# Performance work log

Measured on AMD Instinct MI355X. Metric: run time of the kernel, lower is better.

The kernel has to match this reference:

```python
import jax, jax.numpy as jnp
import numpy as np

C, H, NP = 256, 8, 64      # d_model, nhead, num_prototype
DH, DK = C // H, NP // H   # value head dim, prototype head dim
EPS = 1e-6


def layer_norm(x, g, b, eps=1e-5):
    m = jnp.mean(x, axis=-1, keepdims=True)
    v = jnp.mean((x - m) ** 2, axis=-1, keepdims=True)
    return (x - m) * jax.lax.rsqrt(v + eps) * g + b


def linear_attention(Q, K, V, q_mask=None, kv_mask=None):
    # LoFTR kernelized linear attention, feature map elu(x)+1
    Q = jax.nn.elu(Q) + 1.0
    K = jax.nn.elu(K) + 1.0
    if q_mask is not None:
        Q = Q * q_mask[:, :, None, None].astype(Q.dtype)
    if kv_mask is not None:
        m = kv_mask[:, :, None, None].astype(K.dtype)
        K = K * m
        V = V * m
    v_len = V.shape[1]
    Vn = V / v_len
    KV = jnp.einsum('nshd,nshv->nhdv', K, Vn)                      # [n,h,d,v]
    Z = 1.0 / (jnp.einsum('nlhd,nhd->nlh', Q, K.sum(axis=1)) + EPS)
    return jnp.einsum('nlhd,nhdv,nlh->nlhv', Q, KV, Z) * v_len


def detr_decoder(query, feat, feat_mask, p):
    bs = query.shape[0]
    # query self-attention
    qq = (query @ p['dWqq']).reshape(bs, -1, H, DH)
    qk = (query @ p['dWqk']).reshape(bs, -1, H, DH)
    qv = (query @ p['dWqv']).reshape(bs, -1, H, DH)
    msg = linear_attention(qq, qk, qv, None, None).reshape(bs, -1, C) @ p['dWqm']
    msg = layer_norm(query + msg, p['dln1_g'], p['dln1_b'])
    # prototype cross-attention over feat
    mq = (msg @ p['dWpq']).reshape(bs, -1, H, DH)
    fk = (feat @ p['dWpk']).reshape(bs, -1, H, DH)
    fv = (feat @ p['dWpv']).reshape(bs, -1, H, DH)
    proto = linear_attention(mq, fk, fv, None, feat_mask).reshape(bs, -1, C) @ p['dWpm']
    proto = layer_norm(msg + proto, p['dln2_g'], p['dln2_b'])
    ffn = jax.nn.relu(proto @ p['dWf1']) @ p['dWf2']
    return layer_norm(proto + ffn, p['dln3_g'], p['dln3_b'])


def forward(x, source, x_mask, source_mask, p):
    bs = x.shape[0]
    q = x @ p['Wq']
    k = source @ p['Wk']
    # DETR-style prototype extraction from x
    proto_in = jnp.broadcast_to(p['proto_q'][None], (bs, NP, C))
    prototype = detr_decoder(proto_in, x, x_mask, p)
    pp = prototype @ p['Wqp']
    pk = prototype @ p['Wkp']
    # re-project q/k through prototypes: [n,l,K]
    q = jnp.einsum('nlc,nkc->nlk', q, pp)
    k = jnp.einsum('nsc,nkc->nsk', k, pk)
    q = jnp.where(x_mask[:, :, None], q, -jnp.inf)
    q = jax.nn.softmax(q, axis=1) * jnp.nan_to_num(jax.nn.softmax(q, axis=2))
    k = jnp.where(source_mask[:, :, None], k, -jnp.inf)
    k = jax.nn.softmax(k, axis=1) * jnp.nan_to_num(jax.nn.softmax(k, axis=2))
    q = q.reshape(bs, -1, H, DK)
    k = k.reshape(bs, -1, H, DK)
    v = (source @ p['Wv']).reshape(bs, -1, H, DH)
    msg = linear_attention(q, k, v, x_mask, source_mask)
    msg = msg.reshape(bs, -1, C) @ p['Wmerge']
    msg = layer_norm(msg, p['ln1_g'], p['ln1_b'])
    msg = jax.nn.relu(jnp.concatenate([x, msg], axis=-1) @ p['Wmlp1']) @ p['Wmlp2']
    msg = layer_norm(msg, p['ln2_g'], p['ln2_b'])
    return x + msg


def setup_inputs() -> dict:
    key = jax.random.key(0)
    ks = jax.random.split(key, 24)
    def W(i, shape, scale):
        return jax.random.normal(ks[i], shape, jnp.float32) * scale
    s = 1.0 / np.sqrt(C).astype(np.float32)
    s2 = 1.0 / np.sqrt(2 * C).astype(np.float32)
    B, L, S = 8, 4800, 4800
    ones_c = jnp.ones((C,), jnp.float32)
    zeros_c = jnp.zeros((C,), jnp.float32)
    return {
        'x': W(0, (B, L, C), 1.0),
        'source': W(1, (B, S, C), 1.0),
        'x_mask': jnp.ones((B, L), dtype=bool),
        'source_mask': jnp.ones((B, S), dtype=bool),
        'Wq': W(2, (C, C), s), 'Wk': W(3, (C, C), s), 'Wv': W(4, (C, C), s),
        'Wqp': W(5, (C, C), s), 'Wkp': W(6, (C, C), s),
        'Wmerge': W(7, (C, C), s),
        'Wmlp1': W(8, (2 * C, 2 * C), s2), 'Wmlp2': W(9, (2 * C, C), s2),
        'ln1_g': ones_c, 'ln1_b': zeros_c,
        'ln2_g': ones_c, 'ln2_b': zeros_c,
        'proto_q': W(10, (NP, C), 1.0),
        'dWqq': W(11, (C, C), s), 'dWqk': W(12, (C, C), s),
        'dWqv': W(13, (C, C), s), 'dWqm': W(14, (C, C), s),
        'dln1_g': ones_c, 'dln1_b': zeros_c,
        'dWpq': W(15, (C, C), s), 'dWpk': W(16, (C, C), s),
        'dWpv': W(17, (C, C), s), 'dWpm': W(18, (C, C), s),
        'dln2_g': ones_c, 'dln2_b': zeros_c,
        'dWf1': W(19, (C, C), s), 'dWf2': W(20, (C, C), s),
        'dln3_g': ones_c, 'dln3_b': zeros_c,
    }


def reference(x, source, x_mask, source_mask, Wq, Wk, Wv, Wqp, Wkp, Wmerge,
              Wmlp1, Wmlp2, ln1_g, ln1_b, ln2_g, ln2_b, proto_q,
              dWqq, dWqk, dWqv, dWqm, dln1_g, dln1_b,
              dWpq, dWpk, dWpv, dWpm, dln2_g, dln2_b,
              dWf1, dWf2, dln3_g, dln3_b):
    p = dict(Wq=Wq, Wk=Wk, Wv=Wv, Wqp=Wqp, Wkp=Wkp, Wmerge=Wmerge,
             Wmlp1=Wmlp1, Wmlp2=Wmlp2, ln1_g=ln1_g, ln1_b=ln1_b,
             ln2_g=ln2_g, ln2_b=ln2_b, proto_q=proto_q,
             dWqq=dWqq, dWqk=dWqk, dWqv=dWqv, dWqm=dWqm,
             dln1_g=dln1_g, dln1_b=dln1_b,
             dWpq=dWpq, dWpk=dWpk, dWpv=dWpv, dWpm=dWpm,
             dln2_g=dln2_g, dln2_b=dln2_b,
             dWf1=dWf1, dWf2=dWf2, dln3_g=dln3_g, dln3_b=dln3_b)
    return forward(x, source, x_mask, source_mask, p)
```

## Files before the change

### kernel.cpp

```cpp
#include <hip/hip_runtime.h>
#include <hip/hip_bf16.h>

typedef unsigned short u16;
typedef __bf16 bf16x8 __attribute__((ext_vector_type(8)));
typedef float  f32x4  __attribute__((ext_vector_type(4)));

__device__ __forceinline__ float b2f(u16 u){
  union{ unsigned int i; float f; } a; a.i = ((unsigned int)u)<<16; return a.f;
}
__device__ __forceinline__ u16 f2b(float f){
  __hip_bfloat16 h = __float2bfloat16(f);
  u16 r; __builtin_memcpy(&r, &h, 2); return r;
}
__device__ __forceinline__ int imin(int a,int b){ return a<b?a:b; }

__device__ __forceinline__ void gl_lds16(const void* g, void* l){
  __builtin_amdgcn_global_load_lds(
      (const __attribute__((address_space(1))) void*)g,
      (__attribute__((address_space(3))) void*)l, 16, 0, 0);
}
__device__ __forceinline__ void vm_drain(){
  asm volatile("s_waitcnt vmcnt(0)" ::: "memory");
}
__device__ __forceinline__ void vm_wait4(){
  asm volatile("s_waitcnt vmcnt(4)" ::: "memory");
}

template<int KD, int OUTMODE, bool CAT, int NSEL>
__global__ __launch_bounds__(256) void gemm128(
    const u16* __restrict__ A, const u16* __restrict__ A2, const u16* __restrict__ A3,
    const u16* __restrict__ Wt, const u16* __restrict__ Wt2, const u16* __restrict__ Wt3,
    float* __restrict__ Cf, u16* __restrict__ Cb, u16* __restrict__ Cb2, u16* __restrict__ Cb3,
    int NDIM, int aoff)
{
  __shared__ u16 At[3][128*32];
  __shared__ u16 Bt[3][128*32];
  const int tid = threadIdx.x;
  const int ny = gridDim.y, nz = gridDim.z;
  const int NB = gridDim.x*ny*nz;
  const int L  = blockIdx.x + gridDim.x*(blockIdx.y + ny*blockIdx.z);
  const int cpx = NB >> 3;
  const int wkid = (L & 7)*cpx + (L >> 3);
  const int nc = ny*nz;
  const int bx = wkid / nc;
  const int cc_ = wkid - bx*nc;
  const int by = cc_ % ny;
  const int bz = cc_ / ny;

  const u16* Aa = (NSEL>=3 && bz==2) ? A3 : A;
  const u16* W  = (NSEL>=2 && bz==1) ? Wt2 : ((NSEL>=3 && bz==2) ? Wt3 : Wt);
  u16* Cbo      = (NSEL>=2 && bz==1) ? Cb2 : ((NSEL>=3 && bz==2) ? Cb3 : Cb);
  const int w = tid>>6, lane = tid&63;
  const int q4 = lane>>4, l15 = lane&15;
  const int wr = w>>1, wc = w&1;
  const int rstage = lane>>2;
  const int kcol = (((lane&3) ^ ((lane>>2)&3))<<3);
  const size_t arow0 = (size_t)(aoff + bx*128);
  const int n0 = by*128;

  f32x4 acc[4][4];
  #pragma unroll
  for (int i=0;i<4;i++)
    #pragma unroll
    for (int j=0;j<4;j++){ acc[i][j][0]=0.f; acc[i][j][1]=0.f; acc[i][j][2]=0.f; acc[i][j][3]=0.f; }

  auto stage = [&](int k0, int buf){
    #pragma unroll
    for (int j=0;j<2;j++){
      const int trow = w*32 + j*16 + rstage;
      const u16* ga;
      if (CAT){
        ga = (k0<256) ? (A  + (arow0+trow)*256 + k0 + kcol)
                      : (A2 + (arow0+trow)*256 + (k0-256) + kcol);
      } else {
        ga = Aa + (arow0+trow)*(size_t)KD + k0 + kcol;
      }
      gl_lds16(ga, &At[buf][(w*32+j*16)*32]);
      const u16* gb = W + (size_t)(n0 + trow)*KD + k0 + kcol;
      gl_lds16(gb, &Bt[buf][(w*32+j*16)*32]);
    }
  };

  constexpr int NK = KD/32;
  stage(0, 0);
  stage(32, 1);
  vm_wait4();
  __builtin_amdgcn_s_barrier();
  int cb = 0;
  for (int t=0; t<NK; ++t){
    if (t+2 < NK){
      int sbuf = cb ? cb-1 : 2;
      stage((t+2)*32, sbuf);
    }
    bf16x8 af[4], bv[4];
    #pragma unroll
    for (int i=0;i<4;i++){
      __builtin_memcpy(&af[i], &At[cb][(wr*64 + i*16 + l15)*32 + ((q4^(l15&3))<<3)], 16);
      __builtin_memcpy(&bv[i], &Bt[cb][(wc*64 + i*16 + l15)*32 + ((q4^(l15&3))<<3)], 16);
    }
    #pragma unroll
    for (int i=0;i<4;i++)
      #pragma unroll
      for (int j=0;j<4;j++)
        acc[i][j] = __builtin_amdgcn_mfma_f32_16x16x32_bf16(af[i], bv[j], acc[i][j], 0,0,0);
    if (t+1 < NK){
      if (t+2 < NK) vm_wait4(); else vm_drain();
      __builtin_amdgcn_s_barrier();
      cb = (cb==2)? 0 : cb+1;
    }
  }
  #pragma unroll
  for (int i=0;i<4;i++){
    const int row0 = bx*128 + wr*64 + i*16 + q4*4;
    #pragma unroll
    for (int j=0;j<4;j++){
      const int col = n0 + wc*64 + j*16 + l15;
      #pragma unroll
      for (int r=0;r<4;r++){
        float v = acc[i][j][r];
        size_t idx = (size_t)(row0+r)*NDIM + col;
        if (OUTMODE==0) Cf[idx]=v;
        else if (OUTMODE==1) Cbo[idx]=f2b(v);
        else Cbo[idx]=f2b(v>0.f?v:0.f);
      }
    }
  }
}

__global__ __launch_bounds__(256) void cvt_split2(
    const float* __restrict__ inA, u16* __restrict__ ohA, u16* __restrict__ olA,
    const float* __restrict__ inB, u16* __restrict__ ohB, u16* __restrict__ olB, int n){
  int i = (blockIdx.x*256 + threadIdx.x)*4;
  const float* in; u16 *oh, *ol; int j;
  if (i < n){ in=inA; oh=ohA; ol=olA; j=i; }
  else      { in=inB; oh=ohB; ol=olB; j=i-n; }
  float4 f = *(const float4*)(in+j);
  float v[4]={f.x,f.y,f.z,f.w};
  #pragma unroll
  for (int t=0;t<4;t++){ u16 h=f2b(v[t]); oh[j+t]=h; ol[j+t]=f2b(v[t]-b2f(h)); }
}

__global__ __launch_bounds__(256) void wtrans4(
    const float* __restrict__ W0, const float* __restrict__ W1,
    const float* __restrict__ W2, const float* __restrict__ W3,
    u16* __restrict__ T0, u16* __restrict__ T1,
    u16* __restrict__ T2, u16* __restrict__ T3)
{
  const int g = blockIdx.y;
  const float* W = g==0?W0:(g==1?W1:(g==2?W2:W3));
  u16* T = g==0?T0:(g==1?T1:(g==2?T2:T3));
  int idx = blockIdx.x*256 + threadIdx.x;
  int nn = idx>>8, kk = idx&255;
  T[idx] = f2b(W[(size_t)kk*256 + nn]);
}

__global__ __launch_bounds__(256) void wtrans2(
    const float* __restrict__ W1, u16* __restrict__ T1,
    const float* __restrict__ W2, u16* __restrict__ T2)
{
  int idx = blockIdx.x*256 + threadIdx.x;
  if (idx < 512*512){
    int nn = idx>>9, kk = idx&511;
    T1[idx] = f2b(W1[(size_t)kk*512 + nn]);
  } else {
    int j = idx - 512*512;
    int nn = j>>9, kk = j&511;
    T2[j] = f2b(W2[(size_t)kk*256 + nn]);
  }
}

__global__ __launch_bounds__(256) void warm7(
    const float* __restrict__ W0, const float* __restrict__ W1,
    const float* __restrict__ W2, const float* __restrict__ W3,
    const float* __restrict__ W4, const float* __restrict__ W5,
    const float* __restrict__ W6, float* __restrict__ scratch)
{
  const int slice = blockIdx.x >> 3;
  const int wsel = slice >> 6;
  const int off = ((slice & 63)<<8) + threadIdx.x;
  const float* W = wsel==0?W0:wsel==1?W1:wsel==2?W2:wsel==3?W3:wsel==4?W4:wsel==5?W5:W6;
  float4 v = ((const float4*)W)[off];
  float s = v.x+v.y+v.z+v.w;
  if (s == 1234567.891f) scratch[blockIdx.x] = s;
}

__global__ __launch_bounds__(256) void gemm_logits2(
    const u16* __restrict__ Ah0, const u16* __restrict__ Al0,
    const u16* __restrict__ Bh0, const u16* __restrict__ Bl0,
    float* __restrict__ O0,
    const u16* __restrict__ Ah1, const u16* __restrict__ Al1,
    const u16* __restrict__ Bh1, const u16* __restrict__ Bl1,
    float* __restrict__ O1)
{
  __shared__ u16 SA[3][64*32], SAL[3][64*32], SB[3][64*32], SBL[3][64*32];
  const int tid=threadIdx.x, bx=blockIdx.x;
  const int sel = blockIdx.y;
  const u16* Ah = sel? Ah1:Ah0;  const u16* Al = sel? Al1:Al0;
  const u16* BhT= sel? Bh1:Bh0;  const u16* BlT= sel? Bl1:Bl0;
  float* Out = sel? O1:O0;
  const int w=tid>>6, lane=tid&63, q4=lane>>4, l15=lane&15;
  const int bloc = bx/75;
  const u16* bh_ = BhT + (size_t)bloc*16384;
  const u16* bl_ = BlT + (size_t)bloc*16384;
  const size_t arow0 = (size_t)bx*64;
  const int rsub = lane>>2;
  const int csub = (((lane&3) ^ ((lane>>2)&3))<<3);
  f32x4 acc[4];
  #pragma unroll
  for (int t=0;t<4;t++){ acc[t][0]=0.f; acc[t][1]=0.f; acc[t][2]=0.f; acc[t][3]=0.f; }

  auto stage = [&](int k0, int buf){
    #pragma unroll
    for (int i=0;i<4;i++){
      const int row = i*16 + rsub;
      if (w==0)      gl_lds16(Ah + (arow0+row)*256 + k0 + csub, &SA [buf][i*16*32]);
      else if (w==1) gl_lds16(Al + (arow0+row)*256 + k0 + csub, &SAL[buf][i*16*32]);
      else if (w==2) gl_lds16(bh_ + (size_t)row*256 + k0 + csub, &SB [buf][i*16*32]);
      else           gl_lds16(bl_ + (size_t)row*256 + k0 + csub, &SBL[buf][i*16*32]);
    }
  };

  stage(0, 0);
  stage(32, 1);
  vm_wait4();
  __builtin_amdgcn_s_barrier();
  int cb = 0;
  for (int t=0;t<8;++t){
    if (t+2 < 8){
      int sbuf = cb ? cb-1 : 2;
      stage((t+2)*32, sbuf);
    }
    bf16x8 ah, al;
    __builtin_memcpy(&ah, &SA [cb][(w*16+l15)*32 + ((q4^(l15&3))<<3)], 16);
    __builtin_memcpy(&al, &SAL[cb][(w*16+l15)*32 + ((q4^(l15&3))<<3)], 16);
    #pragma unroll
    for (int nt=0;nt<4;nt++){
      bf16x8 bh, bl;
      __builtin_memcpy(&bh, &SB [cb][(nt*16+l15)*32 + ((q4^(l15&3))<<3)], 16);
      __builtin_memcpy(&bl, &SBL[cb][(nt*16+l15)*32 + ((q4^(l15&3))<<3)], 16);
      acc[nt] = __builtin_amdgcn_mfma_f32_16x16x32_bf16(ah, bh, acc[nt], 0,0,0);
      acc[nt] = __builtin_amdgcn_mfma_f32_16x16x32_bf16(ah, bl, acc[nt], 0,0,0);
      acc[nt] = __builtin_amdgcn_mfma_f32_16x16x32_bf16(al, bh, acc[nt], 0,0,0);
    }
    if (t+1 < 8){
      if (t+2 < 8) vm_wait4(); else vm_drain();
      __builtin_amdgcn_s_barrier();
      cb = (cb==2)? 0 : cb+1;
    }
  }
  #pragma unroll
  for (int nt=0;nt<4;nt++)
    #pragma unroll
    for (int r=0;r<4;r++)
      Out[(arow0 + w*16 + q4*4 + r)*64 + nt*16 + l15] = acc[nt][r];
}

template<int DKT, bool ELU, bool KF32, bool KSM>
__global__ __launch_bounds__(256) void la_reduce_mfma(
    const void* __restrict__ Kv, int kstride, const u16* __restrict__ Vv,
    float* __restrict__ KV, float* __restrict__ Ks, int Skv,
    const float* __restrict__ cmax, const float* __restrict__ csum)
{
  constexpr int PAD = 136;
  constexpr int MROW = (DKT<16)?16:DKT;
  __shared__ u16 Klt[MROW*PAD];
  __shared__ u16 Vlt[32*PAD];
  __shared__ float Ksl[DKT];
  const int tid = threadIdx.x;
  const int bh = blockIdx.y; const int b = bh>>3, h = bh&7;
  const int s0 = blockIdx.x*256;
  if (tid < DKT) Ksl[tid] = 0.f;

  const int w = tid>>6, lane = tid&63, q4 = lane>>4, l15 = lane&15;
  constexpr int NT = (DKT==32)?4:2;
  const int tileid = w % NT;
  const int mt = (DKT==32)? (tileid>>1) : 0;
  const int nt = (DKT==32)? (tileid&1) : tileid;
  constexpr int KPER = (DKT==32)?4:2;
  const int k0w = (w/NT)*KPER;

  const int kd = tid & (DKT-1);
  const int ksrow = tid / DKT;
  const int ksstep = 256/DKT;
  const int vv = tid & 31, vsrow = tid >> 5;

  f32x4 acc; acc[0]=0.f; acc[1]=0.f; acc[2]=0.f; acc[3]=0.f;
  float kacc = 0.f;

  for (int cc=0; cc<2; cc++){
    const int sc0 = s0 + cc*128;
    if constexpr (KSM){
      #pragma unroll
      for (int t=0; t<4; t++){
        int s = ksrow + t*32;
        float xv = 0.f;
        if (sc0+s < Skv){
          const float* rowp = (const float*)Kv + ((size_t)b*Skv + sc0+s)*64;
          float vals[8];
          #pragma unroll
          for (int j=0;j<8;j++) vals[j] = rowp[kd + 8*j];
          float m = vals[0];
          #pragma unroll
          for (int j=1;j<8;j++) m = fmaxf(m, vals[j]);
          #pragma unroll
          for (int off=1;off<8;off<<=1) m = fmaxf(m, __shfl_xor(m, off));
          float ssum = 0.f;
          #pragma unroll
          for (int j=0;j<8;j++) ssum += __expf(vals[j]-m);
          #pragma unroll
          for (int off=1;off<8;off<<=1) ssum += __shfl_xor(ssum, off);
          float vneed = vals[0];
          #pragma unroll
          for (int j=1;j<8;j++) if (h==j) vneed = vals[j];
          const int np = h*8 + kd;
          float cs = __expf(vneed - cmax[(size_t)b*64+np]) / csum[(size_t)b*64+np];
          xv = (__expf(vneed-m)/ssum)*cs + 1.f;
        }
        Klt[kd*PAD + s] = f2b(xv);
        kacc += xv;
      }
    } else {
      #pragma unroll
      for (int t=0; t<DKT/2; t++){
        int s = ksrow + t*ksstep;
        float xv = 0.f;
        if (sc0+s < Skv){
          size_t gi = ((size_t)b*Skv + sc0+s)*kstride + h*DKT + kd;
          float kk = KF32 ? ((const float*)Kv)[gi] : b2f(((const u16*)Kv)[gi]);
          xv = ELU ? (kk>0.f? kk+1.f : __expf(kk)) : kk+1.f;
        }
        Klt[kd*PAD + s] = f2b(xv);
        kacc += xv;
      }
    }
    if (DKT==8){
      for (int i=tid; i<8*128; i+=256){ int rr=8+(i>>7), s=i&127; Klt[rr*PAD+s]=0; }
    }
    #pragma unroll
    for (int t=0; t<16; t++){
      int s = vsrow + t*8;
      u16 raw = 0;
      if (sc0+s < Skv) raw = Vv[((size_t)b*Skv + sc0+s)*256 + h*32 + vv];
      Vlt[vv*PAD + s] = raw;
    }
    __syncthreads();
    #pragma unroll
    for (int kk=0; kk<KPER; kk++){
      int ks = k0w + kk;
      bf16x8 af, bv;
      __builtin_memcpy(&af, &Klt[(mt*16+l15)*PAD + ks*32 + q4*8], 16);
      __builtin_memcpy(&bv, &Vlt[(nt*16+l15)*PAD + ks*32 + q4*8], 16);
      acc = __builtin_amdgcn_mfma_f32_16x16x32_bf16(af, bv, acc, 0,0,0);
    }
    __syncthreads();
  }
  #pragma unroll
  for (int r=0;r<4;r++){
    int row = q4*4 + r;
    if (DKT==32 || row < 8){
      int dg = mt*16 + row;
      atomicAdd(&KV[((size_t)bh*DKT + dg)*32 + nt*16 + l15], acc[r]);
    }
  }
  atomicAdd(&Ksl[kd], kacc);
  __syncthreads();
  if (tid < DKT) atomicAdd(&Ks[(size_t)bh*DKT + tid], Ksl[tid]);
}

__global__ __launch_bounds__(256) void small_gemm3(
    const float* __restrict__ A,
    const float* __restrict__ W0, const float* __restrict__ W1, const float* __restrict__ W2,
    float* __restrict__ O0, float* __restrict__ O1, float* __restrict__ O2,
    int mode, int amask)
{
  __shared__ float Alds[4][256];
  const int g = blockIdx.x>>7;
  const float* W = g==0?W0:(g==1?W1:W2);
  float* Of = g==0?O0:(g==1?O1:O2);
  const int tid=threadIdx.x; const int r0=(blockIdx.x&127)*4;
  for (int i=tid;i<1024;i+=256){ int r=i>>8, c=i&255;
    Alds[r][c]=A[(size_t)((r0+r)&amask)*256+c]; }
  __syncthreads();
  float a0=0.f,a1=0.f,a2=0.f,a3=0.f;
  for (int k=0;k<256;k++){
    float w=W[(size_t)k*256+tid];
    a0+=Alds[0][k]*w; a1+=Alds[1][k]*w; a2+=Alds[2][k]*w; a3+=Alds[3][k]*w;
  }
  float accs[4]={a0,a1,a2,a3};
  #pragma unroll
  for (int r=0;r<4;r++){
    size_t idx=(size_t)(r0+r)*256+tid; float v=accs[r];
    if (mode==1) v = v>0.f?v:0.f;
    Of[idx]=v;
  }
}

template<int R>
__global__ __launch_bounds__(256) void decoder_chain(
    const float* __restrict__ S1, const float* __restrict__ proq,
    const float* __restrict__ KV1, const float* __restrict__ Ks1,
    const float* __restrict__ KV2, const float* __restrict__ Ks2,
    const float* __restrict__ dWqm, const float* __restrict__ dl1g, const float* __restrict__ dl1b,
    const float* __restrict__ dWpq,
    const float* __restrict__ dWpm, const float* __restrict__ dl2g, const float* __restrict__ dl2b,
    const float* __restrict__ dWf1, const float* __restrict__ dWf2,
    const float* __restrict__ dl3g, const float* __restrict__ dl3b,
    const float* __restrict__ Wqp, const float* __restrict__ Wkp,
    float* __restrict__ ppf, float* __restrict__ pkf)
{
  __shared__ float KVl[8*32*32];
  __shared__ float Ksl[8*32];
  __shared__ float rowA[R][256];
  __shared__ float rowB[R][256];
  __shared__ float red[4][R], red2[4][R];
  const int tid = threadIdx.x;
  const int r0g = blockIdx.x*R;
  const int b = r0g >> 6;
  const int h = tid>>5, vv = tid&31;
  const int w_ = tid>>6, ln_ = tid&63;

  auto gemmR = [&](float (*Ain)[256], const float* __restrict__ W, float* out){
    float a[R];
    #pragma unroll
    for (int r=0;r<R;r++) a[r]=0.f;
    float wv[16], wn[16];
    #pragma unroll
    for (int u=0;u<16;u++) wn[u]=0.f;
    #pragma unroll
    for (int u=0;u<16;u++) wv[u]=W[(size_t)u*256+tid];
    for (int k0=0;k0<256;k0+=16){
      if (k0+16<256){
        #pragma unroll
        for (int u=0;u<16;u++) wn[u]=W[(size_t)(k0+16+u)*256+tid];
      }
      #pragma unroll
      for (int u=0;u<16;u++){
        #pragma unroll
        for (int r=0;r<R;r++) a[r]+=Ain[r][k0+u]*wv[u];
      }
      #pragma unroll
      for (int u=0;u<16;u++) wv[u]=wn[u];
    }
    #pragma unroll
    for (int r=0;r<R;r++) out[r]=a[r];
  };
  auto lnR = [&](float* v, const float* __restrict__ g, const float* __restrict__ be,
                 float (*Out)[256]){
    float s[R];
    #pragma unroll
    for (int r=0;r<R;r++) s[r]=v[r];
    #pragma unroll
    for (int off=32;off;off>>=1){
      #pragma unroll
      for (int r=0;r<R;r++) s[r]+=__shfl_xor(s[r],off);
    }
    if (ln_==0){
      #pragma unroll
      for (int r=0;r<R;r++) red[w_][r]=s[r];
    }
    __syncthreads();
    float mean[R];
    #pragma unroll
    for (int r=0;r<R;r++) mean[r]=(red[0][r]+red[1][r]+red[2][r]+red[3][r])*(1.f/256.f);
    float q[R];
    #pragma unroll
    for (int r=0;r<R;r++){ float d=v[r]-mean[r]; q[r]=d*d; }
    #pragma unroll
    for (int off=32;off;off>>=1){
      #pragma unroll
      for (int r=0;r<R;r++) q[r]+=__shfl_xor(q[r],off);
    }
    if (ln_==0){
      #pragma unroll
      for (int r=0;r<R;r++) red2[w_][r]=q[r];
    }
    __syncthreads();
    const float gg=g[tid], bb=be[tid];
    #pragma unroll
    for (int r=0;r<R;r++){
      float var=(red2[0][r]+red2[1][r]+red2[2][r]+red2[3][r])*(1.f/256.f);
      Out[r][tid]=(v[r]-mean[r])*rsqrtf(var+1e-5f)*gg+bb;
    }
    __syncthreads();
  };
  auto applyR = [&](float (*Q)[256], float (*Out)[256]){
    float res[R];
    #pragma unroll
    for (int r=0;r<R;r++){
      float z=0.f,o=0.f;
      #pragma unroll 8
      for (int d=0;d<32;d++){
        float q = Q[r][h*32+d];
        q = q>0.f? q+1.f : __expf(q);
        z += q*Ksl[h*32+d];
        o += q*KVl[(h*32+d)*32+vv];
      }
      res[r]=o/(z+1e-6f);
    }
    __syncthreads();
    #pragma unroll
    for (int r=0;r<R;r++) Out[r][h*32+vv]=res[r];
    __syncthreads();
  };

  for (int i=tid;i<8192;i+=256) KVl[i]=KV1[(size_t)b*8192+i];
  Ksl[tid]=Ks1[(size_t)b*256+tid];
  for (int i=tid;i<R*256;i+=256){ int r=i>>8,c=i&255; rowA[r][c]=S1[(size_t)(r0g+r)*256+c]; }
  __syncthreads();
  applyR(rowA,rowB);
  float v[R], v2[R];
  gemmR(rowB,dWqm,v);
  #pragma unroll
  for (int r=0;r<R;r++) v[r]+=proq[(size_t)((r0g+r)&63)*256+tid];
  lnR(v,dl1g,dl1b,rowA);
  gemmR(rowA,dWpq,v2);
  #pragma unroll
  for (int r=0;r<R;r++) rowB[r][tid]=v2[r];
  for (int i=tid;i<8192;i+=256) KVl[i]=KV2[(size_t)b*8192+i];
  Ksl[tid]=Ks2[(size_t)b*256+tid];
  __syncthreads();
  applyR(rowB,rowB);
  gemmR(rowB,dWpm,v);
  #pragma unroll
  for (int r=0;r<R;r++) v[r]+=rowA[r][tid];
  lnR(v,dl2g,dl2b,rowA);
  gemmR(rowA,dWf1,v);
  #pragma unroll
  for (int r=0;r<R;r++) rowB[r][tid]=v[r]>0.f?v[r]:0.f;
  __syncthreads();
  gemmR(rowB,dWf2,v);
  #pragma unroll
  for (int r=0;r<R;r++) v[r]+=rowA[r][tid];
  lnR(v,dl3g,dl3b,rowA);
  gemmR(rowA,Wqp,v);
  gemmR(rowA,Wkp,v2);
  #pragma unroll
  for (int r=0;r<R;r++){
    ppf[(size_t)(r0g+r)*256+tid]=v[r];
    pkf[(size_t)(r0g+r)*256+tid]=v2[r];
  }
}

__global__ __launch_bounds__(256) void proj_mat2(
    const float* __restrict__ Wa, const float* __restrict__ Pa,
    u16* __restrict__ Mha, u16* __restrict__ Mla,
    const float* __restrict__ Wb, const float* __restrict__ Pb,
    u16* __restrict__ Mhb, u16* __restrict__ Mlb)
{
  __shared__ float PL[64][256];
  const float* W = blockIdx.z? Wb:Wa;
  const float* P = blockIdx.z? Pb:Pa;
  u16* MhT = blockIdx.z? Mhb:Mha;
  u16* MlT = blockIdx.z? Mlb:Mla;
  const int b = blockIdx.x, c0 = blockIdx.y*16, tid = threadIdx.x;
  for (int i=tid;i<16384;i+=256){ int row=i>>8, col=i&255;
    PL[row][col] = P[(size_t)(b*64+row)*256 + col]; }
  __syncthreads();
  const int np = tid&63, cl = tid>>6;
  #pragma unroll
  for (int rr=0;rr<4;rr++){
    int ci = cl + rr*4;
    float acc=0.f;
    for (int j=0;j<256;j++) acc += W[(size_t)(c0+ci)*256+j]*PL[np][j];
    size_t idx = (size_t)b*16384 + (size_t)np*256 + (c0+ci);
    u16 h=f2b(acc); MhT[idx]=h; MlT[idx]=f2b(acc-b2f(h));
  }
}

template<int DKT, bool ELU>
__global__ __launch_bounds__(256) void la_reduce(
    const float* __restrict__ Kv, int kstride, const float* __restrict__ Vv,
    float* __restrict__ KV, float* __restrict__ Ks, int Skv, int clen)
{
  __shared__ float Kl[64*DKT];
  __shared__ float Vl[64*32];
  const int b = blockIdx.y>>3, h = blockIdx.y&7;
  const int tid=threadIdx.x;
  const int s0 = blockIdx.x*clen; const int s1 = imin(s0+clen, Skv);
  const int d0 = tid>>5, vvv = tid&31;
  float acc[DKT/8], kac[DKT/8];
  #pragma unroll
  for (int p=0;p<DKT/8;p++){ acc[p]=0.f; kac[p]=0.f; }
  for (int sc=s0; sc<s1; sc+=64){
    int ns = imin(64, s1-sc);
    for (int i=tid;i<ns*DKT;i+=256){ int s=i/DKT, d=i-s*DKT;
      float xv = Kv[((size_t)b*Skv + sc+s)*kstride + h*DKT + d];
      Kl[s*DKT+d] = ELU ? (xv>0.f? xv+1.f : __expf(xv)) : xv+1.f; }
    for (int i=tid;i<ns*32;i+=256){ int s=i>>5, c=i&31;
      Vl[s*32+c] = Vv[((size_t)b*Skv+sc+s)*256 + h*32 + c]; }
    __syncthreads();
    for (int s=0;s<ns;s++){
      float vval = Vl[s*32+vvv];
      #pragma unroll
      for (int p=0;p<DKT/8;p++){ float kk=Kl[s*DKT + d0+8*p]; acc[p]+=kk*vval; kac[p]+=kk; }
    }
    __syncthreads();
  }
  #pragma unroll
  for (int p=0;p<DKT/8;p++)
    atomicAdd(&KV[(((size_t)b*8+h)*DKT + d0+8*p)*32 + vvv], acc[p]);
  if (vvv==0){
    #pragma unroll
    for (int p=0;p<DKT/8;p++)
      atomicAdd(&Ks[((size_t)b*8+h)*DKT + d0+8*p], kac[p]);
  }
}

template<int DKT, bool ELU, bool OUTBF, bool QSM>
__global__ __launch_bounds__(256) void la_apply(
    const float* __restrict__ Qsrc, const float* __restrict__ KV,
    const float* __restrict__ Ks, int Lq, float* __restrict__ outf, u16* __restrict__ outb,
    const float* __restrict__ cmax, const float* __restrict__ csum)
{
  __shared__ float KVl[8*DKT*32];
  __shared__ float Ksl[8*DKT];
  __shared__ float Ql[16*8*DKT];
  const int b = blockIdx.y; const int r0 = blockIdx.x*16;
  const int tid = threadIdx.x;
  const float* KVb = KV + (size_t)b*8*DKT*32;
  for (int i=tid;i<8*DKT*32;i+=256) KVl[i]=KVb[i];
  for (int i=tid;i<8*DKT;i+=256) Ksl[i]=Ks[(size_t)b*8*DKT + i];
  if constexpr (QSM){
    const int wv = tid>>6, ln = tid&63;
    #pragma unroll
    for (int rr=0;rr<4;rr++){
      const int r = wv*4+rr;
      float v = Qsrc[((size_t)b*Lq + r0 + r)*64 + ln];
      float m = v;
      #pragma unroll
      for (int off=32;off;off>>=1) m = fmaxf(m, __shfl_xor(m,off));
      float e = __expf(v-m);
      float s = e;
      #pragma unroll
      for (int off=32;off;off>>=1) s += __shfl_xor(s,off);
      float cs = __expf(v - cmax[(size_t)b*64+ln]) / csum[(size_t)b*64+ln];
      Ql[r*64+ln] = (e/s)*cs;
    }
  } else {
    for (int i=tid;i<16*8*DKT;i+=256){ int r=i/(8*DKT); int c=i-r*(8*DKT);
        Ql[i] = Qsrc[((size_t)b*Lq + r0 + r)*(8*DKT) + c]; }
  }
  __syncthreads();
  const int h = tid>>5, vv = tid&31;
  for (int r=0;r<16;r++){
    float z=0.f, o=0.f;
    #pragma unroll
    for (int d=0; d<DKT; d++){
      float q = Ql[r*8*DKT + h*DKT + d];
      q = ELU ? (q>0.f? q+1.f : __expf(q)) : q+1.f;
      z += q*Ksl[h*DKT+d];
      o += q*KVl[(h*DKT+d)*32 + vv];
    }
    float res = o/(z+1e-6f);
    size_t idx = ((size_t)b*Lq + r0+r)*256 + h*32+vv;
    if (OUTBF) outb[idx]=f2b(res); else outf[idx]=res;
  }
}

template<int MODE, bool ABF>
__global__ __launch_bounds__(256) void ln_kernel(
  const void* __restrict__ Av, const float* __restrict__ resid,
  const float* __restrict__ g, const float* __restrict__ be,
  float* __restrict__ Of, u16* __restrict__ Ob, const float* __restrict__ xadd,
  float* __restrict__ Ox)
{
  const int tid = threadIdx.x;
  const size_t row = (size_t)blockIdx.x*4 + (tid>>6);
  const int lane = tid&63;
  const int c0 = lane<<2;
  const size_t gi = row*256 + c0;
  float v[4];
  if (MODE==1 || ABF){
    ushort4 u = *(const ushort4*)((const u16*)Av + gi);
    v[0]=b2f(u.x); v[1]=b2f(u.y); v[2]=b2f(u.z); v[3]=b2f(u.w);
  } else {
    float4 f = *(const float4*)((const float*)Av + gi);
    v[0]=f.x; v[1]=f.y; v[2]=f.z; v[3]=f.w;
  }
  if (MODE==0){
    float4 r = *(const float4*)(resid + gi);
    v[0]+=r.x; v[1]+=r.y; v[2]+=r.z; v[3]+=r.w;
  }
  float s = v[0]+v[1]+v[2]+v[3];
  #pragma unroll
  for (int off=32;off;off>>=1) s += __shfl_xor(s,off);
  const float mean = s*(1.f/256.f);
  float d[4]; float qq=0.f;
  #pragma unroll
  for (int i=0;i<4;i++){ d[i]=v[i]-mean; qq += d[i]*d[i]; }
  #pragma unroll
  for (int off=32;off;off>>=1) qq += __shfl_xor(qq,off);
  const float rstd = rsqrtf(qq*(1.f/256.f)+1e-5f);
  const float4 gv = *(const float4*)(g+c0);
  const float4 bv = *(const float4*)(be+c0);
  float y[4];
  y[0]=d[0]*rstd*gv.x+bv.x; y[1]=d[1]*rstd*gv.y+bv.y;
  y[2]=d[2]*rstd*gv.z+bv.z; y[3]=d[3]*rstd*gv.w+bv.w;
  if (MODE==0){
    *(float4*)(Of+gi) = make_float4(y[0],y[1],y[2],y[3]);
  } else if (MODE==1){
    ushort4 o; o.x=f2b(y[0]); o.y=f2b(y[1]); o.z=f2b(y[2]); o.w=f2b(y[3]);
    *(ushort4*)(Ob+gi)=o;
  } else {
    const float4 xa = *(const float4*)(xadd+gi);
    *(float4*)(Ox+gi) = make_float4(xa.x+y[0], xa.y+y[1], xa.z+y[2], xa.w+y[3]);
  }
}

__global__ __launch_bounds__(256) void col_stats(
    const float* __restrict__ logits0, float* __restrict__ cmax0, float* __restrict__ csum0,
    const float* __restrict__ logits1, float* __restrict__ cmax1, float* __restrict__ csum1)
{
  int np = blockIdx.x, b = blockIdx.y;
  const float* logits = blockIdx.z? logits1:logits0;
  float* cmax = blockIdx.z? cmax1:cmax0;
  float* csum = blockIdx.z? csum1:csum0;
  const float* base = logits + ((size_t)b*4800)*64 + np;
  int tid = threadIdx.x;
  float vloc[19];
  float m = -3.0e38f;
  #pragma unroll
  for (int i=0;i<19;i++){ int l = tid + i*256;
    float v = (l<4800)? base[(size_t)l*64] : -3.0e38f;
    vloc[i]=v; m = fmaxf(m,v); }
  #pragma unroll
  for (int off=32;off;off>>=1) m = fmaxf(m, __shfl_xor(m,off));
  __shared__ float red[4], red2[4];
  int w = tid>>6, ln = tid&63;
  if (ln==0) red[w]=m;
  __syncthreads();
  m = fmaxf(fmaxf(red[0],red[1]), fmaxf(red[2],red[3]));
  float s=0.f;
  #pragma unroll
  for (int i=0;i<19;i++){ int l = tid + i*256; if (l<4800) s += __expf(vloc[i]-m); }
  #pragma unroll
  for (int off=32;off;off>>=1) s += __shfl_xor(s,off);
  if (ln==0) red2[w]=s;
  __syncthreads();
  s = red2[0]+red2[1]+red2[2]+red2[3];
  if (tid==0){ cmax[b*64+np]=m; csum[b*64+np]=s; }
}

extern "C" void kernel_launch(void* const* d_in, const int* in_sizes, int n_in,
                              void* d_out, int out_size, void* d_ws, size_t ws_size,
                              hipStream_t stream) {
  (void)in_sizes; (void)n_in; (void)out_size; (void)ws_size;
  const float* x    = (const float*)d_in[0];
  const float* srcp = (const float*)d_in[1];
  const float* Wq   = (const float*)d_in[4];
  const float* Wk   = (const float*)d_in[5];
  const float* Wv   = (const float*)d_in[6];
  const float* Wqp  = (const float*)d_in[7];
  const float* Wkp  = (const float*)d_in[8];
  const float* Wmg  = (const float*)d_in[9];
  const float* Wm1  = (const float*)d_in[10];
  const float* Wm2  = (const float*)d_in[11];
  const float* ln1g = (const float*)d_in[12];
  const float* ln1b = (const float*)d_in[13];
  const float* ln2g = (const float*)d_in[14];
  const float* ln2b = (const float*)d_in[15];
  const float* proq = (const float*)d_in[16];
  const float* dWqq = (const float*)d_in[17];
  const float* dWqk = (const float*)d_in[18];
  const float* dWqv = (const float*)d_in[19];
  const float* dWqm = (const float*)d_in[20];
  const float* dl1g = (const float*)d_in[21];
  const float* dl1b = (const float*)d_in[22];
  const float* dWpq = (const float*)d_in[23];
  const float* dWpk = (const float*)d_in[24];
  const float* dWpv = (const float*)d_in[25];
  const float* dWpm = (const float*)d_in[26];
  const float* dWf1 = (const float*)d_in[29];
  const float* dWf2 = (const float*)d_in[30];
  const float* dl3g = (const float*)d_in[31];
  const float* dl3b = (const float*)d_in[32];
  const float* dl2g = (const float*)d_in[27];
  const float* dl2b = (const float*)d_in[28];

  char* p=(char*)d_ws;
  auto alloc=[&](size_t n)->char*{ char* r=p; p+=((n+255)&~(size_t)255); return r; };
  u16* xb  = (u16*)alloc(19660800);
  u16* xlo = (u16*)alloc(19660800);
  u16* sb  = (u16*)alloc(19660800);
  u16* slo = (u16*)alloc(19660800);
  u16* bufA= (u16*)alloc(19660800);
  u16* bufB= (u16*)alloc(19660800);
  u16* v0b = (u16*)alloc(19660800);
  u16* msg1b=(u16*)alloc(19660800);
  u16* h1  = (u16*)alloc(39321600);
  u16* mlp2b=(u16*)alloc(19660800);
  float* qsm=(float*)alloc(9830400);
  float* ksm=(float*)alloc(9830400);
  u16* dWpkT=(u16*)alloc(131072); u16* dWpvT=(u16*)alloc(131072);
  u16* WvT  =(u16*)alloc(131072); u16* WmgT =(u16*)alloc(131072);
  u16* Wm1T =(u16*)alloc(524288); u16* Wm2T =(u16*)alloc(262144);
  float* S0=(float*)alloc(524288); float* S1=(float*)alloc(524288);
  float* S2=(float*)alloc(524288); float* S3=(float*)alloc(524288);
  float* S4=(float*)alloc(524288); float* S5=(float*)alloc(524288);
  float* ppf=(float*)alloc(524288); float* pkf=(float*)alloc(524288);
  u16* Mqh=(u16*)alloc(262144); u16* Mql=(u16*)alloc(262144);
  u16* Mkh=(u16*)alloc(262144); u16* Mkl=(u16*)alloc(262144);
  char* z0=p;
  float* KV1=(float*)alloc(262144); float* Ks1=(float*)alloc(8192);
  float* KV2=(float*)alloc(262144); float* Ks2=(float*)alloc(8192);
  float* KVm=(float*)alloc(65536);  float* Ksm=(float*)alloc(2048);
  char* z1=p;
  float* cmq=(float*)alloc(2048); float* csq=(float*)alloc(2048);
  float* cmk=(float*)alloc(2048); float* csk=(float*)alloc(2048);
  (void)S4; (void)S5;

  u16* fk=bufA;
  u16* fv=bufB; u16* msg0b=bufB;
  float* dof=(float*)d_out;

  hipMemsetAsync(z0, 0, (size_t)(z1-z0), stream);

  dim3 blk(256);
  cvt_split2<<<dim3(19200),blk,0,stream>>>(x, xb, xlo, srcp, sb, slo, 9830400);
  wtrans4<<<dim3(256,4),blk,0,stream>>>(dWpk,dWpv,Wv,Wmg, dWpkT,dWpvT,WvT,WmgT);
  wtrans2<<<dim3(1536),blk,0,stream>>>(Wm1, Wm1T, Wm2, Wm2T);
  gemm128<256,1,false,3><<<dim3(300,2,3),blk,0,stream>>>(
      xb,nullptr,sb, dWpkT,dWpvT,WvT, nullptr, fk,fv,v0b, 256,0);
  la_reduce_mfma<32,true,false,false><<<dim3(19,64),blk,0,stream>>>(
      fk,256,fv,KV2,Ks2,4800,nullptr,nullptr);
  small_gemm3<<<dim3(384),blk,0,stream>>>(proq,dWqq,dWqk,dWqv,S1,S2,S3,0,63);
  la_reduce<32,true><<<dim3(1,64),blk,0,stream>>>(S2,256,S3,KV1,Ks1,64,64);
  warm7<<<dim3(3584),blk,0,stream>>>(dWqm,dWpq,dWpm,dWf1,dWf2,Wqp,Wkp,S0);
  decoder_chain<2><<<dim3(256),blk,0,stream>>>(
      S1,proq, KV1,Ks1, KV2,Ks2,
      dWqm,dl1g,dl1b, dWpq, dWpm,dl2g,dl2b, dWf1,dWf2,dl3g,dl3b,
      Wqp,Wkp, ppf,pkf);
  proj_mat2<<<dim3(8,16,2),blk,0,stream>>>(Wq,ppf,Mqh,Mql, Wk,pkf,Mkh,Mkl);
  gemm_logits2<<<dim3(600,2),blk,0,stream>>>(xb,xlo,Mqh,Mql,qsm, sb,slo,Mkh,Mkl,ksm);
  col_stats<<<dim3(64,8,2),blk,0,stream>>>(qsm,cmq,csq, ksm,cmk,csk);
  la_reduce_mfma<8,false,true,true><<<dim3(19,64),blk,0,stream>>>(
      ksm,64,v0b,KVm,Ksm,4800,cmk,csk);
  la_apply<8,false,true,true><<<dim3(300,8),blk,0,stream>>>(
      qsm,KVm,Ksm,4800,nullptr,msg0b,cmq,csq);
  gemm128<256,1,false,1><<<dim3(300,2),blk,0,stream>>>(
      msg0b,nullptr,nullptr, WmgT,nullptr,nullptr, nullptr, msg1b,nullptr,nullptr, 256,0);
  ln_kernel<1,false><<<dim3(9600),blk,0,stream>>>(msg1b,nullptr,ln1g,ln1b,nullptr,msg1b,nullptr,nullptr);
  gemm128<512,2,true,1><<<dim3(300,4),blk,0,stream>>>(
      xb,msg1b,nullptr, Wm1T,nullptr,nullptr, nullptr, h1,nullptr,nullptr, 512,0);
  gemm128<512,1,false,1><<<dim3(300,2),blk,0,stream>>>(
      h1,nullptr,nullptr, Wm2T,nullptr,nullptr, nullptr, mlp2b,nullptr,nullptr, 256,0);
  ln_kernel<2,true><<<dim3(9600),blk,0,stream>>>(mlp2b,nullptr,ln2g,ln2b,nullptr,nullptr,x,dof);
}
```

Measured before the change: 528.3 us.

## Split decoder chain to one row per block and fuse final two projections

The decoder_chain launch changes from two rows per block on 256 blocks to one row per block on 512 blocks, spreading the serial per-row GEMM/LayerNorm chain over more CUs. The final Wqp and Wkp projections are merged into one pass that streams both weight matrices together, so the activation row is read once. The second KV/Ks load into LDS is moved earlier so it sits before the first gemm rather than after the dWpq gemm. More blocks means the weight matrices are re-read from cache more times overall.

```diff
diff --git a/kernel.cpp b/kernel.cpp
--- a/kernel.cpp
+++ b/kernel.cpp
@@ -444,6 +444,33 @@
     #pragma unroll
     for (int r=0;r<R;r++) out[r]=a[r];
   };
+  auto gemmR2 = [&](float (*Ain)[256], const float* __restrict__ Wa,
+                    const float* __restrict__ Wb, float* oa, float* ob){
+    float a[R], bacc[R];
+    #pragma unroll
+    for (int r=0;r<R;r++){ a[r]=0.f; bacc[r]=0.f; }
+    float wa[8], wb[8], na[8], nb[8];
+    #pragma unroll
+    for (int u=0;u<8;u++){ wa[u]=Wa[(size_t)u*256+tid]; wb[u]=Wb[(size_t)u*256+tid]; }
+    for (int k0=0;k0<256;k0+=8){
+      if (k0+8<256){
+        #pragma unroll
+        for (int u=0;u<8;u++){ na[u]=Wa[(size_t)(k0+8+u)*256+tid]; nb[u]=Wb[(size_t)(k0+8+u)*256+tid]; }
+      }
+      #pragma unroll
+      for (int u=0;u<8;u++){
+        #pragma unroll
+        for (int r=0;r<R;r++){
+          float av = Ain[r][k0+u];
+          a[r]+=av*wa[u]; bacc[r]+=av*wb[u];
+        }
+      }
+      #pragma unroll
+      for (int u=0;u<8;u++){ wa[u]=na[u]; wb[u]=nb[u]; }
+    }
+    #pragma unroll
+    for (int r=0;r<R;r++){ oa[r]=a[r]; ob[r]=bacc[r]; }
+  };
   auto lnR = [&](float* v, const float* __restrict__ g, const float* __restrict__ be,
                  float (*Out)[256]){
     float s[R];
@@ -508,6 +535,8 @@
   for (int i=tid;i<R*256;i+=256){ int r=i>>8,c=i&255; rowA[r][c]=S1[(size_t)(r0g+r)*256+c]; }
   __syncthreads();
   applyR(rowA,rowB);
+  for (int i=tid;i<8192;i+=256) KVl[i]=KV2[(size_t)b*8192+i];
+  Ksl[tid]=Ks2[(size_t)b*256+tid];
   float v[R], v2[R];
   gemmR(rowB,dWqm,v);
   #pragma unroll
@@ -516,8 +545,6 @@
   gemmR(rowA,dWpq,v2);
   #pragma unroll
   for (int r=0;r<R;r++) rowB[r][tid]=v2[r];
-  for (int i=tid;i<8192;i+=256) KVl[i]=KV2[(size_t)b*8192+i];
-  Ksl[tid]=Ks2[(size_t)b*256+tid];
   __syncthreads();
   applyR(rowB,rowB);
   gemmR(rowB,dWpm,v);
@@ -532,8 +559,7 @@
   #pragma unroll
   for (int r=0;r<R;r++) v[r]+=rowA[r][tid];
   lnR(v,dl3g,dl3b,rowA);
-  gemmR(rowA,Wqp,v);
-  gemmR(rowA,Wkp,v2);
+  gemmR2(rowA,Wqp,Wkp,v,v2);
   #pragma unroll
   for (int r=0;r<R;r++){
     ppf[(size_t)(r0g+r)*256+tid]=v[r];
@@ -826,7 +852,7 @@
   small_gemm3<<<dim3(384),blk,0,stream>>>(proq,dWqq,dWqk,dWqv,S1,S2,S3,0,63);
   la_reduce<32,true><<<dim3(1,64),blk,0,stream>>>(S2,256,S3,KV1,Ks1,64,64);
   warm7<<<dim3(3584),blk,0,stream>>>(dWqm,dWpq,dWpm,dWf1,dWf2,Wqp,Wkp,S0);
-  decoder_chain<2><<<dim3(256),blk,0,stream>>>(
+  decoder_chain<1><<<dim3(512),blk,0,stream>>>(
       S1,proq, KV1,Ks1, KV2,Ks2,
       dWqm,dl1g,dl1b, dWpq, dWpm,dl2g,dl2b, dWf1,dWf2,dl3g,dl3b,
       Wqp,Wkp, ppf,pkf);
```

New measurement: 521.9 us (median of 2 runs). Within noise of the previous version (-1.2%).

## Split decoder chain to one row per block with split-K GEMV reduction

Applied to the files above, without the earlier changes.

The decoder chain kernel now handles one prototype row per block instead of two, doubling the grid to 512 blocks. Each GEMV splits K across the four waves and combines partial sums through a shared-memory buffer. The final Wqp/Wkp projections are fused into one pass over both weights, and the KV2 load into LDS is moved earlier. The aim is to shorten the serial dependency chain per block and use more CUs, at the cost of extra barriers and more total weight reads across blocks.

```diff
diff --git a/kernel.cpp b/kernel.cpp
--- a/kernel.cpp
+++ b/kernel.cpp
@@ -395,7 +395,6 @@
   }
 }
 
-template<int R>
 __global__ __launch_bounds__(256) void decoder_chain(
     const float* __restrict__ S1, const float* __restrict__ proq,
     const float* __restrict__ KV1, const float* __restrict__ Ks1,
@@ -410,135 +409,137 @@
 {
   __shared__ float KVl[8*32*32];
   __shared__ float Ksl[8*32];
-  __shared__ float rowA[R][256];
-  __shared__ float rowB[R][256];
-  __shared__ float red[4][R], red2[4][R];
+  __shared__ float rowA[256];
+  __shared__ float rowB[256];
+  __shared__ float red[4], red2[4];
+  __shared__ float gred[4][256];
   const int tid = threadIdx.x;
-  const int r0g = blockIdx.x*R;
+  const int r0g = blockIdx.x;
   const int b = r0g >> 6;
   const int h = tid>>5, vv = tid&31;
   const int w_ = tid>>6, ln_ = tid&63;
 
-  auto gemmR = [&](float (*Ain)[256], const float* __restrict__ W, float* out){
-    float a[R];
-    #pragma unroll
-    for (int r=0;r<R;r++) a[r]=0.f;
+  auto gemmS = [&](const float* Ain, const float* __restrict__ W, float& out){
+    const int kb = w_*64;
+    float a0=0.f,a1=0.f,a2=0.f,a3=0.f;
     float wv[16], wn[16];
     #pragma unroll
     for (int u=0;u<16;u++) wn[u]=0.f;
     #pragma unroll
-    for (int u=0;u<16;u++) wv[u]=W[(size_t)u*256+tid];
-    for (int k0=0;k0<256;k0+=16){
-      if (k0+16<256){
+    for (int u=0;u<16;u++) wv[u]=W[(size_t)(kb+u)*256+tid];
+    #pragma unroll
+    for (int kc=0;kc<64;kc+=16){
+      if (kc<48){
         #pragma unroll
-        for (int u=0;u<16;u++) wn[u]=W[(size_t)(k0+16+u)*256+tid];
+        for (int u=0;u<16;u++) wn[u]=W[(size_t)(kb+kc+16+u)*256+tid];
       }
       #pragma unroll
-      for (int u=0;u<16;u++){
+      for (int u=0;u<16;u+=4){
+        a0+=Ain[kb+kc+u  ]*wv[u  ];
+        a1+=Ain[kb+kc+u+1]*wv[u+1];
+        a2+=Ain[kb+kc+u+2]*wv[u+2];
+        a3+=Ain[kb+kc+u+3]*wv[u+3];
+      }
+      #pragma unroll
+      for (int u=0;u<16;u++) wv[u]=wn[u];
+    }
+    gred[w_][tid]=(a0+a1)+(a2+a3);
+    __syncthreads();
+    out = (gred[0][tid]+gred[1][tid])+(gred[2][tid]+gred[3][tid]);
+    __syncthreads();
+  };
+  auto gemmS2 = [&](const float* Ain, const float* __restrict__ Wa,
+                    const float* __restrict__ Wb, float& oa, float& ob){
+    const int kb = w_*64;
+    float a0=0.f,a1=0.f,b0=0.f,b1=0.f;
+    float wa[8], wb[8], na[8], nb[8];
+    #pragma unroll
+    for (int u=0;u<8;u++){ na[u]=0.f; nb[u]=0.f; }
+    #pragma unroll
+    for (int u=0;u<8;u++){ wa[u]=Wa[(size_t)(kb+u)*256+tid]; wb[u]=Wb[(size_t)(kb+u)*256+tid]; }
+    #pragma unroll
+    for (int kc=0;kc<64;kc+=8){
+      if (kc<56){
         #pragma unroll
-        for (int r=0;r<R;r++) a[r]+=Ain[r][k0+u]*wv[u];
+        for (int u=0;u<8;u++){ na[u]=Wa[(size_t)(kb+kc+8+u)*256+tid]; nb[u]=Wb[(size_t)(kb+kc+8+u)*256+tid]; }
       }
       #pragma unroll
-      for (int u=0;u<16;u++) wv[u]=wn[u];
-    }
-    #pragma unroll
-    for (int r=0;r<R;r++) out[r]=a[r];
+      for (int u=0;u<8;u+=2){
+        float av0=Ain[kb+kc+u], av1=Ain[kb+kc+u+1];
+        a0+=av0*wa[u]; a1+=av1*wa[u+1];
+        b0+=av0*wb[u]; b1+=av1*wb[u+1];
+      }
+      #pragma unroll
+      for (int u=0;u<8;u++){ wa[u]=na[u]; wb[u]=nb[u]; }
+    }
+    gred[w_][tid]=a0+a1;
+    __syncthreads();
+    oa = (gred[0][tid]+gred[1][tid])+(gred[2][tid]+gred[3][tid]);
+    __syncthreads();
+    gred[w_][tid]=b0+b1;
+    __syncthreads();
+    ob = (gred[0][tid]+gred[1][tid])+(gred[2][tid]+gred[3][tid]);
+    __syncthreads();
   };
-  auto lnR = [&](float* v, const float* __restrict__ g, const float* __restrict__ be,
-                 float (*Out)[256]){
-    float s[R];
-    #pragma unroll
-    for (int r=0;r<R;r++) s[r]=v[r];
-    #pragma unroll
-    for (int off=32;off;off>>=1){
-      #pragma unroll
-      for (int r=0;r<R;r++) s[r]+=__shfl_xor(s[r],off);
-    }
-    if (ln_==0){
-      #pragma unroll
-      for (int r=0;r<R;r++) red[w_][r]=s[r];
-    }
-    __syncthreads();
-    float mean[R];
-    #pragma unroll
-    for (int r=0;r<R;r++) mean[r]=(red[0][r]+red[1][r]+red[2][r]+red[3][r])*(1.f/256.f);
-    float q[R];
-    #pragma unroll
-    for (int r=0;r<R;r++){ float d=v[r]-mean[r]; q[r]=d*d; }
-    #pragma unroll
-    for (int off=32;off;off>>=1){
-      #pragma unroll
-      for (int r=0;r<R;r++) q[r]+=__shfl_xor(q[r],off);
-    }
-    if (ln_==0){
-      #pragma unroll
-      for (int r=0;r<R;r++) red2[w_][r]=q[r];
-    }
-    __syncthreads();
-    const float gg=g[tid], bb=be[tid];
-    #pragma unroll
-    for (int r=0;r<R;r++){
-      float var=(red2[0][r]+red2[1][r]+red2[2][r]+red2[3][r])*(1.f/256.f);
-      Out[r][tid]=(v[r]-mean[r])*rsqrtf(var+1e-5f)*gg+bb;
-    }
+  auto lnS = [&](float v, const float* __restrict__ g, const float* __restrict__ be,
+                 float* Out){
+    float s=v;
+    #pragma unroll
+    for (int off=32;off;off>>=1) s+=__shfl_xor(s,off);
+    if (ln_==0) red[w_]=s;
+    __syncthreads();
+    float mean=(red[0]+red[1]+red[2]+red[3])*(1.f/256.f);
+    float d=v-mean; float q=d*d;
+    #pragma unroll
+    for (int off=32;off;off>>=1) q+=__shfl_xor(q,off);
+    if (ln_==0) red2[w_]=q;
+    __syncthreads();
+    float var=(red2[0]+red2[1]+red2[2]+red2[3])*(1.f/256.f);
+    Out[tid]=d*rsqrtf(var+1e-5f)*g[tid]+be[tid];
     __syncthreads();
   };
-  auto applyR = [&](float (*Q)[256], float (*Out)[256]){
-    float res[R];
-    #pragma unroll
-    for (int r=0;r<R;r++){
-      float z=0.f,o=0.f;
-      #pragma unroll 8
-      for (int d=0;d<32;d++){
-        float q = Q[r][h*32+d];
-        q = q>0.f? q+1.f : __expf(q);
-        z += q*Ksl[h*32+d];
-        o += q*KVl[(h*32+d)*32+vv];
-      }
-      res[r]=o/(z+1e-6f);
-    }
-    __syncthreads();
-    #pragma unroll
-    for (int r=0;r<R;r++) Out[r][h*32+vv]=res[r];
+  auto applyS = [&](float* Q, float* Out){
+    float z=0.f,o=0.f;
+    #pragma unroll 8
+    for (int d=0;d<32;d++){
+      float q = Q[h*32+d];
+      q = q>0.f? q+1.f : __expf(q);
+      z += q*Ksl[h*32+d];
+      o += q*KVl[(h*32+d)*32+vv];
+    }
+    float res=o/(z+1e-6f);
+    __syncthreads();
+    Out[h*32+vv]=res;
     __syncthreads();
   };
 
   for (int i=tid;i<8192;i+=256) KVl[i]=KV1[(size_t)b*8192+i];
   Ksl[tid]=Ks1[(size_t)b*256+tid];
-  for (int i=tid;i<R*256;i+=256){ int r=i>>8,c=i&255; rowA[r][c]=S1[(size_t)(r0g+r)*256+c]; }
+  rowA[tid]=S1[(size_t)r0g*256+tid];
   __syncthreads();
-  applyR(rowA,rowB);
-  float v[R], v2[R];
-  gemmR(rowB,dWqm,v);
-  #pragma unroll
-  for (int r=0;r<R;r++) v[r]+=proq[(size_t)((r0g+r)&63)*256+tid];
-  lnR(v,dl1g,dl1b,rowA);
-  gemmR(rowA,dWpq,v2);
-  #pragma unroll
-  for (int r=0;r<R;r++) rowB[r][tid]=v2[r];
+  applyS(rowA,rowB);
   for (int i=tid;i<8192;i+=256) KVl[i]=KV2[(size_t)b*8192+i];
   Ksl[tid]=Ks2[(size_t)b*256+tid];
+  float v, v2;
+  gemmS(rowB,dWqm,v);
+  v += proq[(size_t)(r0g&63)*256+tid];
+  lnS(v,dl1g,dl1b,rowA);
+  gemmS(rowA,dWpq,v2);
+  rowB[tid]=v2;
   __syncthreads();
-  applyR(rowB,rowB);
-  gemmR(rowB,dWpm,v);
-  #pragma unroll
-  for (int r=0;r<R;r++) v[r]+=rowA[r][tid];
-  lnR(v,dl2g,dl2b,rowA);
-  gemmR(rowA,dWf1,v);
-  #pragma unroll
-  for (int r=0;r<R;r++) rowB[r][tid]=v[r]>0.f?v[r]:0.f;
+  applyS(rowB,rowB);
+  gemmS(rowB,dWpm,v);
+  v += rowA[tid];
+  lnS(v,dl2g,dl2b,rowA);
+  gemmS(rowA,dWf1,v);
+  rowB[tid]=v>0.f?v:0.f;
   __syncthreads();
-  gemmR(rowB,dWf2,v);
-  #pragma unroll
-  for (int r=0;r<R;r++) v[r]+=rowA[r][tid];
-  lnR(v,dl3g,dl3b,rowA);
-  gemmR(rowA,Wqp,v);
-  gemmR(rowA,Wkp,v2);
-  #pragma unroll
-  for (int r=0;r<R;r++){
-    ppf[(size_t)(r0g+r)*256+tid]=v[r];
-    pkf[(size_t)(r0g+r)*256+tid]=v2[r];
-  }
+  gemmS(rowB,dWf2,v);
+  v += rowA[tid];
+  lnS(v,dl3g,dl3b,rowA);
+  gemmS2(rowA,Wqp,Wkp,v,v2);
+  ppf[(size_t)r0g*256+tid]=v;
+  pkf[(size_t)r0g*256+tid]=v2;
 }
 
 __global__ __launch_bounds__(256) void proj_mat2(
@@ -826,7 +827,7 @@
   small_gemm3<<<dim3(384),blk,0,stream>>>(proq,dWqq,dWqk,dWqv,S1,S2,S3,0,63);
   la_reduce<32,true><<<dim3(1,64),blk,0,stream>>>(S2,256,S3,KV1,Ks1,64,64);
   warm7<<<dim3(3584),blk,0,stream>>>(dWqm,dWpq,dWpm,dWf1,dWf2,Wqp,Wkp,S0);
-  decoder_chain<2><<<dim3(256),blk,0,stream>>>(
+  decoder_chain<<<dim3(512),blk,0,stream>>>(
       S1,proq, KV1,Ks1, KV2,Ks2,
       dWqm,dl1g,dl1b, dWpq, dWpm,dl2g,dl2b, dWf1,dWf2,dl3g,dl3b,
       Wqp,Wkp, ppf,pkf);
```

New measurement: 585.2 us. 1.11x slower.
